# Kernel optimization log

Hardware: AMD Instinct MI355X
Metric: run time of the kernel (lower is better)

Reference implementation:

```python
import jax, jax.numpy as jnp
import numpy as np

N = 500_000   # total nodes
D = 256       # in_dim
G = 1024      # num graphs (segments)
H = max(32, D // 2)  # gate hidden = 128
L = D // 2    # local pool dim = 128


def setup_inputs() -> dict:
    key = jax.random.key(0)
    ks = jax.random.split(key, 8)
    x = jax.random.normal(ks[0], (N, D), dtype=jnp.float32)
    batch = jnp.sort(jax.random.randint(ks[1], (N,), 0, G, dtype=jnp.int32))
    s = 0.02
    w1 = jax.random.normal(ks[2], (D, H), dtype=jnp.float32) * s
    b1 = jnp.zeros((H,), dtype=jnp.float32)
    w2 = jax.random.normal(ks[3], (H, 1), dtype=jnp.float32) * s
    b2 = jnp.zeros((1,), dtype=jnp.float32)
    lp_w = jax.random.normal(ks[4], (D, L), dtype=jnp.float32) * s
    lp_b = jnp.zeros((L,), dtype=jnp.float32)
    return {"x": x, "batch": batch, "w1": w1, "b1": b1, "w2": w2,
            "b2": b2, "lp_w": lp_w, "lp_b": lp_b}


def reference(x, batch, w1, b1, w2, b2, lp_w, lp_b):
    # segment counts (guard empty segments)
    ones = jnp.ones((x.shape[0],), dtype=x.dtype)
    cnt = jax.ops.segment_sum(ones, batch, num_segments=G)
    cnt = jnp.maximum(cnt, 1.0)[:, None]                      # [G,1]

    # mean pool
    mean_p = jax.ops.segment_sum(x, batch, num_segments=G) / cnt

    # max pool
    max_p = jax.ops.segment_max(x, batch, num_segments=G)

    # global attention pool: gate MLP -> per-segment softmax -> weighted sum
    # (Dropout is identity at inference.)
    h = jax.nn.gelu(x @ w1 + b1, approximate=False)           # [N,H]
    gate = (h @ w2 + b2)[:, 0]                                # [N]
    gmax = jax.ops.segment_max(gate, batch, num_segments=G)   # [G]
    e = jnp.exp(gate - gmax[batch])                           # [N]
    denom = jax.ops.segment_sum(e, batch, num_segments=G)     # [G]
    a = e / denom[batch]                                      # [N] softmax per graph
    att_p = jax.ops.segment_sum(a[:, None] * x, batch, num_segments=G)

    # local MLP pool then mean
    local = jax.nn.gelu(x @ lp_w + lp_b, approximate=False)   # [N,L]
    local_mean = jax.ops.segment_sum(local, batch, num_segments=G) / cnt

    return jnp.concatenate([mean_p, max_p, att_p, local_mean], axis=-1)  # [G, 3D + D//2]
```

## Files before the change

kernel.cpp:

```cpp
#include <hip/hip_runtime.h>
#include <hip/hip_bf16.h>
#include <float.h>
#include <math.h>


typedef __bf16 bf16;
typedef __bf16 bf16x8 __attribute__((ext_vector_type(8)));
typedef float f32x4 __attribute__((ext_vector_type(4)));

#define D 256
#define HDIM 128
#define LDIM 128
#define ROWS 16
#define XPAD 260
#define SPLIT 4

__device__ __forceinline__ float gelu_f(float v) {
    return 0.5f * v * (1.0f + erff(v * 0.70710678118654752f));
}

__global__ __launch_bounds__(256) void k_prep(const float* __restrict__ w1,
                                              const float* __restrict__ lpw,
                                              bf16* __restrict__ w1T,
                                              bf16* __restrict__ lpT) {
    int t = blockIdx.x * 256 + threadIdx.x;
    if (t < HDIM * D) {
        int n = t >> 8;
        int k = t & 255;
        w1T[t] = (bf16)w1[k * HDIM + n];
        lpT[t] = (bf16)lpw[k * LDIM + n];
    }
}

__global__ __launch_bounds__(256) void k_bounds(const int* __restrict__ batch,
                                                int* __restrict__ segstart,
                                                int N, int G) {
    int i = blockIdx.x * 256 + threadIdx.x;
    if (i >= N) return;
    int b = batch[i];
    if (i == 0) {
        for (int g = 0; g <= b; ++g) segstart[g] = 0;
    } else {
        int p = batch[i - 1];
        for (int g = p + 1; g <= b; ++g) segstart[g] = i;
    }
    if (i == N - 1) {
        for (int g = b + 1; g <= G; ++g) segstart[g] = N;
    }
}

__global__ __launch_bounds__(256)
void k_fused(const float* __restrict__ x, const int* __restrict__ segstart,
             const bf16* __restrict__ w1T, const float* __restrict__ b1,
             const float* __restrict__ w2, const float* __restrict__ b2,
             const bf16* __restrict__ lpT, const float* __restrict__ lpb,
             float* __restrict__ psum, float* __restrict__ pmax,
             float* __restrict__ patt, float* __restrict__ pls,
             float* __restrict__ pscal)
{
    __shared__ float xf[ROWS][XPAD];
    __shared__ float gpart[4][16];

    const int blk  = blockIdx.x;
    const int g    = blk >> 2;
    const int part = blk & 3;
    const int tid  = threadIdx.x;
    const int wave = tid >> 6;
    const int lane = tid & 63;
    const int quad = lane >> 4;
    const int l16  = lane & 15;

    const int gs = segstart[g], ge = segstart[g + 1];
    const int cnt = ge - gs;
    const int per = (cnt + SPLIT - 1) >> 2;
    const int start = gs + part * per;
    const int end   = min(start + per, ge);

    const int c0 = wave * 32 + l16;
    const int c1 = c0 + 16;
    const float b1c0 = b1[c0], b1c1 = b1[c1];
    const float w2c0 = w2[c0], w2c1 = w2[c1];
    const float lb0  = lpb[c0], lb1 = lpb[c1];
    const float b2c  = b2[0];
    const bf16* wb0 = w1T + c0 * D;
    const bf16* wb1 = w1T + c1 * D;
    const bf16* pb0 = lpT + c0 * D;
    const bf16* pb1 = lpT + c1 * D;

    float msum0=0.f, msum1=0.f, msum2=0.f, msum3=0.f;
    float mmax0=-FLT_MAX, mmax1=-FLT_MAX, mmax2=-FLT_MAX, mmax3=-FLT_MAX;
    float asum0=0.f, asum1=0.f, asum2=0.f, asum3=0.f;
    float ls0=0.f, ls1=0.f;
    float m_run = -FLT_MAX, denom = 0.f;

    for (int base = start; base < end; base += ROWS) {
        const int vr = min(ROWS, end - base);
        const float* xb = x + (long)base * D + (lane << 2);

        if (vr == ROWS) {
            #pragma unroll
            for (int it = 0; it < 4; ++it) {
                const int row = it * 4 + wave;
                const float4 t4 = *(const float4*)(xb + row * D);
                msum0 += t4.x; msum1 += t4.y; msum2 += t4.z; msum3 += t4.w;
                mmax0 = fmaxf(mmax0, t4.x); mmax1 = fmaxf(mmax1, t4.y);
                mmax2 = fmaxf(mmax2, t4.z); mmax3 = fmaxf(mmax3, t4.w);
                f32x4 v; v[0]=t4.x; v[1]=t4.y; v[2]=t4.z; v[3]=t4.w;
                *(f32x4*)(&xf[row][lane << 2]) = v;
            }
        } else {
            #pragma unroll
            for (int it = 0; it < 4; ++it) {
                const int row = it * 4 + wave;
                f32x4 v = {0.f, 0.f, 0.f, 0.f};
                if (row < vr) {
                    const float4 t4 = *(const float4*)(xb + row * D);
                    msum0 += t4.x; msum1 += t4.y; msum2 += t4.z; msum3 += t4.w;
                    mmax0 = fmaxf(mmax0, t4.x); mmax1 = fmaxf(mmax1, t4.y);
                    mmax2 = fmaxf(mmax2, t4.z); mmax3 = fmaxf(mmax3, t4.w);
                    v[0]=t4.x; v[1]=t4.y; v[2]=t4.z; v[3]=t4.w;
                }
                *(f32x4*)(&xf[row][lane << 2]) = v;
            }
        }
        __syncthreads();

        const f32x4 zf = {0.f, 0.f, 0.f, 0.f};
        f32x4 h0 = zf, h1 = zf, l0 = zf, l1 = zf;
        #pragma unroll 1
        for (int kt = 0; kt < 8; ++kt) {
            const int k0 = kt * 32 + quad * 8;
            const bf16x8 bw0v = *(const bf16x8*)(wb0 + k0);
            const bf16x8 bw1v = *(const bf16x8*)(wb1 + k0);
            const bf16x8 bp0v = *(const bf16x8*)(pb0 + k0);
            const bf16x8 bp1v = *(const bf16x8*)(pb1 + k0);
            const float* xp = &xf[l16][k0];
            const f32x4 fa = *(const f32x4*)(xp);
            const f32x4 fb = *(const f32x4*)(xp + 4);
            bf16x8 a;
            a[0]=(bf16)fa[0]; a[1]=(bf16)fa[1]; a[2]=(bf16)fa[2]; a[3]=(bf16)fa[3];
            a[4]=(bf16)fb[0]; a[5]=(bf16)fb[1]; a[6]=(bf16)fb[2]; a[7]=(bf16)fb[3];
            h0 = __builtin_amdgcn_mfma_f32_16x16x32_bf16(a, bw0v, h0, 0, 0, 0);
            h1 = __builtin_amdgcn_mfma_f32_16x16x32_bf16(a, bw1v, h1, 0, 0, 0);
            l0 = __builtin_amdgcn_mfma_f32_16x16x32_bf16(a, bp0v, l0, 0, 0, 0);
            l1 = __builtin_amdgcn_mfma_f32_16x16x32_bf16(a, bp1v, l1, 0, 0, 0);
        }

        #pragma unroll
        for (int r = 0; r < 4; ++r) {
            float v = gelu_f(h0[r] + b1c0) * w2c0
                    + gelu_f(h1[r] + b1c1) * w2c1;
            v += __shfl_down(v, 8, 16);
            v += __shfl_down(v, 4, 16);
            v += __shfl_down(v, 2, 16);
            v += __shfl_down(v, 1, 16);
            if (l16 == 0) gpart[wave][quad * 4 + r] = v;
        }
        __syncthreads();

        float gv = -FLT_MAX;
        if (lane < vr)
            gv = gpart[0][lane] + gpart[1][lane] + gpart[2][lane] + gpart[3][lane] + b2c;
        float cm = gv;
        #pragma unroll
        for (int off = 32; off > 0; off >>= 1) cm = fmaxf(cm, __shfl_xor(cm, off));
        const float m_new = fmaxf(m_run, cm);
        const float fr = expf(m_run - m_new);
        const float ew = (lane < vr) ? expf(gv - m_new) : 0.f;
        float se = ew;
        #pragma unroll
        for (int off = 32; off > 0; off >>= 1) se += __shfl_xor(se, off);
        denom = denom * fr + se;
        m_run = m_new;

        #pragma unroll
        for (int r = 0; r < 4; ++r) {
            if (quad * 4 + r < vr) {
                ls0 += gelu_f(l0[r] + lb0);
                ls1 += gelu_f(l1[r] + lb1);
            }
        }

        asum0 *= fr; asum1 *= fr; asum2 *= fr; asum3 *= fr;
        #pragma unroll
        for (int it = 0; it < 4; ++it) {
            const int row = it * 4 + wave;
            const float e = __shfl(ew, row);
            const f32x4 v = *(const f32x4*)(&xf[row][lane << 2]);
            asum0 += e * v[0]; asum1 += e * v[1];
            asum2 += e * v[2]; asum3 += e * v[3];
        }
        __syncthreads();
    }

    ls0 += __shfl_xor(ls0, 16); ls0 += __shfl_xor(ls0, 32);
    ls1 += __shfl_xor(ls1, 16); ls1 += __shfl_xor(ls1, 32);

    float* red = &xf[0][0];
    const int cb = (wave << 8) + (lane << 2);
    {
        f32x4 v0 = {msum0, msum1, msum2, msum3};
        f32x4 v1 = {asum0, asum1, asum2, asum3};
        f32x4 v2 = {mmax0, mmax1, mmax2, mmax3};
        *(f32x4*)(&red[cb])        = v0;
        *(f32x4*)(&red[1024 + cb]) = v1;
        *(f32x4*)(&red[2048 + cb]) = v2;
    }
    if (quad == 0) {
        pls[(long)blk * LDIM + c0] = ls0;
        pls[(long)blk * LDIM + c1] = ls1;
    }
    if (tid == 0) {
        const int pcnt = (end > start) ? (end - start) : 0;
        pscal[(long)blk * 4 + 0] = m_run;
        pscal[(long)blk * 4 + 1] = denom;
        pscal[(long)blk * 4 + 2] = (float)pcnt;
    }
    __syncthreads();
    {
        const int col = tid;
        const float s  = red[col]        + red[256 + col]  + red[512 + col]  + red[768 + col];
        const float a  = red[1024 + col] + red[1280 + col] + red[1536 + col] + red[1792 + col];
        const float mx = fmaxf(fmaxf(red[2048 + col], red[2304 + col]),
                               fmaxf(red[2560 + col], red[2816 + col]));
        psum[(long)blk * 256 + col] = s;
        patt[(long)blk * 256 + col] = a;
        pmax[(long)blk * 256 + col] = mx;
    }
}

__global__ __launch_bounds__(256) void k_merge(
    const float* __restrict__ psum, const float* __restrict__ pmax,
    const float* __restrict__ patt, const float* __restrict__ pls,
    const float* __restrict__ pscal, float* __restrict__ out)
{
    const int g   = blockIdx.x;
    const int tid = threadIdx.x;
    __shared__ float sm[SPLIT], sd[SPLIT], sc[SPLIT];
    if (tid < SPLIT) {
        sm[tid] = pscal[(long)(g * SPLIT + tid) * 4 + 0];
        sd[tid] = pscal[(long)(g * SPLIT + tid) * 4 + 1];
        sc[tid] = pscal[(long)(g * SPLIT + tid) * 4 + 2];
    }
    __syncthreads();
    const float M   = fmaxf(fmaxf(sm[0], sm[1]), fmaxf(sm[2], sm[3]));
    const float cnt = sc[0] + sc[1] + sc[2] + sc[3];
    float w[SPLIT];
    float denom = 0.f;
    #pragma unroll
    for (int p = 0; p < SPLIT; ++p) {
        w[p] = expf(sm[p] - M);
        denom += sd[p] * w[p];
    }
    const float inv  = 1.0f / fmaxf(cnt, 1.0f);
    const float invd = (denom > 0.f) ? 1.0f / denom : 0.f;
    const long  o    = (long)g * 896;
    const long  pb   = (long)g * SPLIT * 256;
    {
        const int col = tid;
        float s = 0.f, a = 0.f, mx = -FLT_MAX;
        #pragma unroll
        for (int p = 0; p < SPLIT; ++p) {
            s += psum[pb + p * 256 + col];
            mx = fmaxf(mx, pmax[pb + p * 256 + col]);
            a += patt[pb + p * 256 + col] * w[p];
        }
        out[o + col]       = s * inv;
        out[o + 256 + col] = (cnt > 0.f) ? mx : -INFINITY;
        out[o + 512 + col] = a * invd;
    }
    if (tid < 128) {
        const long lb = (long)g * SPLIT * 128;
        float s = 0.f;
        #pragma unroll
        for (int p = 0; p < SPLIT; ++p) s += pls[lb + p * 128 + tid];
        out[o + 768 + tid] = s * inv;
    }
}

extern "C" void kernel_launch(void* const* d_in, const int* in_sizes, int n_in,
                              void* d_out, int out_size, void* d_ws, size_t ws_size,
                              hipStream_t stream) {
    const float* x   = (const float*)d_in[0];
    const int* batch = (const int*)d_in[1];
    const float* w1  = (const float*)d_in[2];
    const float* b1  = (const float*)d_in[3];
    const float* w2  = (const float*)d_in[4];
    const float* b2  = (const float*)d_in[5];
    const float* lpw = (const float*)d_in[6];
    const float* lpb = (const float*)d_in[7];
    float* out = (float*)d_out;

    const int N = in_sizes[0] / D;
    const int G = out_size / 896;
    const int NB = SPLIT * G;

    char* ws = (char*)d_ws;
    size_t off = 0;
    auto alloc = [&](size_t bytes) { void* p = ws + off; off = (off + bytes + 255) & ~(size_t)255; return p; };
    bf16*  w1T      = (bf16*)alloc((size_t)HDIM * D * sizeof(bf16));
    bf16*  lpT      = (bf16*)alloc((size_t)LDIM * D * sizeof(bf16));
    int*   segstart = (int*)alloc((size_t)(G + 1) * sizeof(int));
    float* psum     = (float*)alloc((size_t)NB * 256 * sizeof(float));
    float* pmax     = (float*)alloc((size_t)NB * 256 * sizeof(float));
    float* patt     = (float*)alloc((size_t)NB * 256 * sizeof(float));
    float* pls      = (float*)alloc((size_t)NB * 128 * sizeof(float));
    float* pscal    = (float*)alloc((size_t)NB * 4 * sizeof(float));

    k_prep<<<(HDIM * D + 255) / 256, 256, 0, stream>>>(w1, lpw, w1T, lpT);
    k_bounds<<<(N + 255) / 256, 256, 0, stream>>>(batch, segstart, N, G);
    k_fused<<<NB, 256, 0, stream>>>(x, segstart, w1T, b1, w2, b2, lpT, lpb,
                                    psum, pmax, patt, pls, pscal);
    k_merge<<<G, 256, 0, stream>>>(psum, pmax, patt, pls, pscal, out);
}
```

Measured before the change: 1.067 ms.

## Double-buffer x tiles via direct global-to-LDS DMA with XOR swizzle and fast GELU

```diff
diff --git a/kernel.cpp b/kernel.cpp
--- a/kernel.cpp
+++ b/kernel.cpp
@@ -12,11 +12,28 @@
 #define HDIM 128
 #define LDIM 128
 #define ROWS 16
-#define XPAD 260
 #define SPLIT 4
 
 __device__ __forceinline__ float gelu_f(float v) {
-    return 0.5f * v * (1.0f + erff(v * 0.70710678118654752f));
+    const float z  = v * 0.70710678118654752f;
+    const float az = fabsf(z);
+    const float t  = __builtin_amdgcn_rcpf(1.0f + 0.3275911f * az);
+    float p = 1.061405429f;
+    p = p * t - 1.453152027f;
+    p = p * t + 1.421413741f;
+    p = p * t - 0.284496736f;
+    p = p * t + 0.254829592f;
+    p = p * t;
+    const float e    = __expf(-z * z);
+    const float erfa = 1.0f - p * e;
+    const float erfs = copysignf(erfa, z);
+    return 0.5f * v * (1.0f + erfs);
+}
+
+__device__ __forceinline__ void dma_row16(const float* src, const float* lds_dst) {
+    __builtin_amdgcn_global_load_lds(
+        (const __attribute__((address_space(1))) void*)src,
+        (__attribute__((address_space(3))) void*)lds_dst, 16, 0, 0);
 }
 
 __global__ __launch_bounds__(256) void k_prep(const float* __restrict__ w1,
@@ -49,7 +66,7 @@
     }
 }
 
-__global__ __launch_bounds__(256)
+__global__ __launch_bounds__(256, 3)
 void k_fused(const float* __restrict__ x, const int* __restrict__ segstart,
              const bf16* __restrict__ w1T, const float* __restrict__ b1,
              const float* __restrict__ w2, const float* __restrict__ b2,
@@ -58,7 +75,7 @@
              float* __restrict__ patt, float* __restrict__ pls,
              float* __restrict__ pscal)
 {
-    __shared__ float xf[ROWS][XPAD];
+    __shared__ float xbuf[2][ROWS][D];
     __shared__ float gpart[4][16];
 
     const int blk  = blockIdx.x;
@@ -69,12 +86,14 @@
     const int lane = tid & 63;
     const int quad = lane >> 4;
     const int l16  = lane & 15;
+    const int s7   = l16 & 7;
 
     const int gs = segstart[g], ge = segstart[g + 1];
     const int cnt = ge - gs;
     const int per = (cnt + SPLIT - 1) >> 2;
     const int start = gs + part * per;
     const int end   = min(start + per, ge);
+    const int nchunk = (end > start) ? ((end - start + ROWS - 1) / ROWS) : 0;
 
     const int c0 = wave * 32 + l16;
     const int c1 = c0 + 16;
@@ -87,43 +106,33 @@
     const bf16* pb0 = lpT + c0 * D;
     const bf16* pb1 = lpT + c1 * D;
 
-    float msum0=0.f, msum1=0.f, msum2=0.f, msum3=0.f;
-    float mmax0=-FLT_MAX, mmax1=-FLT_MAX, mmax2=-FLT_MAX, mmax3=-FLT_MAX;
-    float asum0=0.f, asum1=0.f, asum2=0.f, asum3=0.f;
-    float ls0=0.f, ls1=0.f;
+    f32x4 msum = {0.f, 0.f, 0.f, 0.f};
+    f32x4 asum = {0.f, 0.f, 0.f, 0.f};
+    f32x4 mmax = {-FLT_MAX, -FLT_MAX, -FLT_MAX, -FLT_MAX};
+    float ls0 = 0.f, ls1 = 0.f;
     float m_run = -FLT_MAX, denom = 0.f;
 
-    for (int base = start; base < end; base += ROWS) {
-        const int vr = min(ROWS, end - base);
-        const float* xb = x + (long)base * D + (lane << 2);
-
-        if (vr == ROWS) {
-            #pragma unroll
-            for (int it = 0; it < 4; ++it) {
-                const int row = it * 4 + wave;
-                const float4 t4 = *(const float4*)(xb + row * D);
-                msum0 += t4.x; msum1 += t4.y; msum2 += t4.z; msum3 += t4.w;
-                mmax0 = fmaxf(mmax0, t4.x); mmax1 = fmaxf(mmax1, t4.y);
-                mmax2 = fmaxf(mmax2, t4.z); mmax3 = fmaxf(mmax3, t4.w);
-                f32x4 v; v[0]=t4.x; v[1]=t4.y; v[2]=t4.z; v[3]=t4.w;
-                *(f32x4*)(&xf[row][lane << 2]) = v;
-            }
-        } else {
-            #pragma unroll
-            for (int it = 0; it < 4; ++it) {
-                const int row = it * 4 + wave;
-                f32x4 v = {0.f, 0.f, 0.f, 0.f};
-                if (row < vr) {
-                    const float4 t4 = *(const float4*)(xb + row * D);
-                    msum0 += t4.x; msum1 += t4.y; msum2 += t4.z; msum3 += t4.w;
-                    mmax0 = fmaxf(mmax0, t4.x); mmax1 = fmaxf(mmax1, t4.y);
-                    mmax2 = fmaxf(mmax2, t4.z); mmax3 = fmaxf(mmax3, t4.w);
-                    v[0]=t4.x; v[1]=t4.y; v[2]=t4.z; v[3]=t4.w;
-                }
-                *(f32x4*)(&xf[row][lane << 2]) = v;
-            }
-        }
-        __syncthreads();
+    if (nchunk > 0) {
+        const int vr0 = min(ROWS, end - start);
+        #pragma unroll
+        for (int it = 0; it < 4; ++it) {
+            const int row = it * 4 + wave;
+            if (row < vr0)
+                dma_row16(x + (long)(start + row) * D + ((lane ^ (row & 7)) << 2),
+                          &xbuf[0][row][0]);
+        }
+    }
+
+    int cur = 0;
+    for (int ck = 0; ck < nchunk; ++ck) {
+        const int base = start + ck * ROWS;
+        const int vr   = min(ROWS, end - base);
+
+        asm volatile("s_waitcnt vmcnt(0)" ::: "memory");
+        __builtin_amdgcn_s_barrier();
+        __builtin_amdgcn_sched_barrier(0);
+
+        float (*xb)[D] = xbuf[cur];
 
         const f32x4 zf = {0.f, 0.f, 0.f, 0.f};
         f32x4 h0 = zf, h1 = zf, l0 = zf, l1 = zf;
@@ -134,9 +143,12 @@
             const bf16x8 bw1v = *(const bf16x8*)(wb1 + k0);
             const bf16x8 bp0v = *(const bf16x8*)(pb0 + k0);
             const bf16x8 bp1v = *(const bf16x8*)(pb1 + k0);
-            const float* xp = &xf[l16][k0];
-            const f32x4 fa = *(const f32x4*)(xp);
-            const f32x4 fb = *(const f32x4*)(xp + 4);
+            const int cch = kt * 8 + quad * 2;
+            const int p0  = cch ^ s7;
+            const int p1  = p0 ^ 1;
+            const float* xp = &xb[l16][0];
+            const f32x4 fa = *(const f32x4*)(xp + p0 * 4);
+            const f32x4 fb = *(const f32x4*)(xp + p1 * 4);
             bf16x8 a;
             a[0]=(bf16)fa[0]; a[1]=(bf16)fa[1]; a[2]=(bf16)fa[2]; a[3]=(bf16)fa[3];
             a[4]=(bf16)fb[0]; a[5]=(bf16)fb[1]; a[6]=(bf16)fb[2]; a[7]=(bf16)fb[3];
@@ -144,6 +156,18 @@
             h1 = __builtin_amdgcn_mfma_f32_16x16x32_bf16(a, bw1v, h1, 0, 0, 0);
             l0 = __builtin_amdgcn_mfma_f32_16x16x32_bf16(a, bp0v, l0, 0, 0, 0);
             l1 = __builtin_amdgcn_mfma_f32_16x16x32_bf16(a, bp1v, l1, 0, 0, 0);
+        }
+
+        if (ck + 1 < nchunk) {
+            const int nb  = base + ROWS;
+            const int vrn = min(ROWS, end - nb);
+            #pragma unroll
+            for (int it = 0; it < 4; ++it) {
+                const int row = it * 4 + wave;
+                if (row < vrn)
+                    dma_row16(x + (long)(nb + row) * D + ((lane ^ (row & 7)) << 2),
+                              &xbuf[cur ^ 1][row][0]);
+            }
         }
 
         #pragma unroll
@@ -156,7 +180,10 @@
             v += __shfl_down(v, 1, 16);
             if (l16 == 0) gpart[wave][quad * 4 + r] = v;
         }
-        __syncthreads();
+
+        asm volatile("s_waitcnt lgkmcnt(0)" ::: "memory");
+        __builtin_amdgcn_s_barrier();
+        __builtin_amdgcn_sched_barrier(0);
 
         float gv = -FLT_MAX;
         if (lane < vr)
@@ -165,8 +192,8 @@
         #pragma unroll
         for (int off = 32; off > 0; off >>= 1) cm = fmaxf(cm, __shfl_xor(cm, off));
         const float m_new = fmaxf(m_run, cm);
-        const float fr = expf(m_run - m_new);
-        const float ew = (lane < vr) ? expf(gv - m_new) : 0.f;
+        const float fr = __expf(m_run - m_new);
+        const float ew = (lane < vr) ? __expf(gv - m_new) : 0.f;
         float se = ew;
         #pragma unroll
         for (int off = 32; off > 0; off >>= 1) se += __shfl_xor(se, off);
@@ -181,31 +208,32 @@
             }
         }
 
-        asum0 *= fr; asum1 *= fr; asum2 *= fr; asum3 *= fr;
+        asum[0] *= fr; asum[1] *= fr; asum[2] *= fr; asum[3] *= fr;
         #pragma unroll
         for (int it = 0; it < 4; ++it) {
             const int row = it * 4 + wave;
-            const float e = __shfl(ew, row);
-            const f32x4 v = *(const f32x4*)(&xf[row][lane << 2]);
-            asum0 += e * v[0]; asum1 += e * v[1];
-            asum2 += e * v[2]; asum3 += e * v[3];
-        }
-        __syncthreads();
+            if (row < vr) {
+                const float e = __shfl(ew, row);
+                const f32x4 v = *(const f32x4*)(&xb[row][(lane ^ (row & 7)) << 2]);
+                msum[0] += v[0]; msum[1] += v[1]; msum[2] += v[2]; msum[3] += v[3];
+                mmax[0] = fmaxf(mmax[0], v[0]); mmax[1] = fmaxf(mmax[1], v[1]);
+                mmax[2] = fmaxf(mmax[2], v[2]); mmax[3] = fmaxf(mmax[3], v[3]);
+                asum[0] += e * v[0]; asum[1] += e * v[1];
+                asum[2] += e * v[2]; asum[3] += e * v[3];
+            }
+        }
+        cur ^= 1;
     }
 
     ls0 += __shfl_xor(ls0, 16); ls0 += __shfl_xor(ls0, 32);
     ls1 += __shfl_xor(ls1, 16); ls1 += __shfl_xor(ls1, 32);
 
-    float* red = &xf[0][0];
+    __syncthreads();
+    float* red = &xbuf[0][0][0];
     const int cb = (wave << 8) + (lane << 2);
-    {
-        f32x4 v0 = {msum0, msum1, msum2, msum3};
-        f32x4 v1 = {asum0, asum1, asum2, asum3};
-        f32x4 v2 = {mmax0, mmax1, mmax2, mmax3};
-        *(f32x4*)(&red[cb])        = v0;
-        *(f32x4*)(&red[1024 + cb]) = v1;
-        *(f32x4*)(&red[2048 + cb]) = v2;
-    }
+    *(f32x4*)(&red[cb])        = msum;
+    *(f32x4*)(&red[1024 + cb]) = asum;
+    *(f32x4*)(&red[2048 + cb]) = mmax;
     if (quad == 0) {
         pls[(long)blk * LDIM + c0] = ls0;
         pls[(long)blk * LDIM + c1] = ls1;
```

Result: no change. 1.070 ms (+0.3%).
